# Optimization experiments

Hardware: AMD Instinct MI355X
Metric: run time of the kernel (lower is better)

Reference implementation:

```python
import jax, jax.numpy as jnp
import numpy as np

N, H, D = 32768, 32, 64


def mobius_addition(x, y, c):
    xy_dot = jnp.sum(x * y, axis=-1, keepdims=True)
    x_norm_sq = jnp.sum(x ** 2, axis=-1, keepdims=True)
    y_norm_sq = jnp.sum(y ** 2, axis=-1, keepdims=True)
    num = (1 + 2 * c * xy_dot + c * y_norm_sq) * x + (1 - c * x_norm_sq) * y
    den = 1 + 2 * c * xy_dot + c * c * x_norm_sq * y_norm_sq
    return num / den


def exp_map(x, v, c):
    v_norm = jnp.linalg.norm(v, axis=-1, keepdims=True)
    sqrt_c = jnp.sqrt(c)
    second = jnp.tanh(sqrt_c * v_norm / 2) * v / (sqrt_c * v_norm)
    return mobius_addition(x, second, c)


def log_map(x, y, c):
    add = mobius_addition(-x, y, c)
    add_norm = jnp.linalg.norm(add, axis=-1, keepdims=True)
    sqrt_c = jnp.sqrt(c)
    return 2 / sqrt_c * jnp.arctanh(sqrt_c * add_norm) * add / add_norm


def setup_inputs() -> dict:
    key = jax.random.key(0)
    ks = jax.random.split(key, 5)
    s = 0.1 / np.sqrt(D)  # keep embeddings well inside the Poincare ball (norm ~0.1)
    return {
        "current_emb": jax.random.normal(ks[0], (N, D), jnp.float32) * s,
        "history": jax.random.normal(ks[1], (H, N, D), jnp.float32) * s,
        "curvature": jnp.ones((1,), jnp.float32),
        "Wq": jax.random.normal(ks[2], (D, D), jnp.float32) / np.sqrt(D),
        "bq": jnp.zeros((D,), jnp.float32),
        "Wk": jax.random.normal(ks[3], (D, D), jnp.float32) / np.sqrt(D),
        "bk": jnp.zeros((D,), jnp.float32),
        "attn_vec": jax.random.normal(ks[4], (D, 1), jnp.float32),
    }


def reference(current_emb, history, curvature, Wq, bq, Wk, bk, attn_vec):
    c = curvature.reshape(())
    origin = jnp.zeros((1, D), current_emb.dtype)
    # log map at origin: hyperbolic -> tangent space
    tangent_current = log_map(origin, current_emb, c)          # [N, D]
    tangent_history = log_map(origin, history, c)              # [H, N, D] (origin broadcasts)
    query = tangent_current @ Wq.T + bq                        # [N, D]
    keys = jnp.einsum('hnd,ed->hne', tangent_history, Wk) + bk  # [H, N, D]
    scores = jnp.tanh(query[None, :, :] + keys)                # [H, N, D]
    weights = scores @ attn_vec                                # [H, N, 1]
    weights = jax.nn.softmax(weights, axis=0)
    weighted_sum = jnp.sum(weights * tangent_history, axis=0)  # [N, D]
    context = exp_map(origin, weighted_sum, c)                 # [N, D]
    return context
```

## Files before the change

### kernel.cpp

```cpp
#include <hip/hip_runtime.h>
#include <math.h>

#define NTOK 32768
#define HH 32
#define DD 64
#define TPB 16
#define NBLK (NTOK / TPB)

typedef float f4 __attribute__((ext_vector_type(4)));
typedef short bf16x8 __attribute__((ext_vector_type(8)));

__device__ __forceinline__ float rcpf_(float x) { return __builtin_amdgcn_rcpf(x); }

__device__ __forceinline__ float tanh_f(float x) {
    float t = __expf(x + x);
    return (t - 1.f) * rcpf_(t + 1.f);
}

__device__ __forceinline__ float tanh_poly(float x) {
    float x2 = x * x;
    float t = fmaf(x2, -0.05396825f, 0.13333333f);
    t = fmaf(x2, t, -0.33333333f);
    t = fmaf(x2, t, 1.f);
    return x * t;
}

__device__ __forceinline__ float logmap_f(float x) {
    float u = __logf((1.f + x) * rcpf_(1.f - x));
    return (x > 1e-4f) ? u * rcpf_(x) : 2.f;
}

__device__ __forceinline__ bf16x8 hi8(f4 a, f4 b) {
    bf16x8 r;
#pragma unroll
    for (int j = 0; j < 4; ++j) {
        r[j]     = (short)(__float_as_uint(a[j]) >> 16);
        r[j + 4] = (short)(__float_as_uint(b[j]) >> 16);
    }
    return r;
}
__device__ __forceinline__ bf16x8 lo8(f4 a, f4 b) {
    bf16x8 r;
#pragma unroll
    for (int j = 0; j < 4; ++j) {
        float ah = __uint_as_float(__float_as_uint(a[j]) & 0xFFFF0000u);
        float bh = __uint_as_float(__float_as_uint(b[j]) & 0xFFFF0000u);
        r[j]     = (short)(__float_as_uint(a[j] - ah) >> 16);
        r[j + 4] = (short)(__float_as_uint(b[j] - bh) >> 16);
    }
    return r;
}

__device__ __forceinline__ void load4(const float* base, int l15, int quad, f4 yv[4]) {
    const float* r = base + l15 * DD + 8 * quad;
    yv[0] = *(const f4*)(r);
    yv[1] = *(const f4*)(r + 4);
    yv[2] = *(const f4*)(r + 32);
    yv[3] = *(const f4*)(r + 36);
}

__device__ __forceinline__ float tangent_factor(const f4 yv[4], float sc) {
    f4 s4 = yv[0]*yv[0] + yv[1]*yv[1] + yv[2]*yv[2] + yv[3]*yv[3];
    float n = s4[0] + s4[1] + s4[2] + s4[3];
    n += __shfl_xor(n, 16);
    n += __shfl_xor(n, 32);
    return logmap_f(sc * sqrtf(n));
}

__global__ __launch_bounds__(256, 2) void hyp_attn_v10(
    const float* __restrict__ cur, const float* __restrict__ hist,
    const float* __restrict__ curv, const float* __restrict__ Wq,
    const float* __restrict__ bq, const float* __restrict__ Wk,
    const float* __restrict__ bk, const float* __restrict__ av,
    float* __restrict__ out)
{
    __shared__ float oBuf[4][TPB][68];
    __shared__ float lBuf[4][TPB];

    const int tid  = threadIdx.x;
    const int wv   = tid >> 6;
    const int lane = tid & 63;
    const int l15  = lane & 15;
    const int quad = lane >> 4;
    const int bb   = blockIdx.x;
    const int tok0 = bb * TPB;

    const float sc = sqrtf(curv[0]);
    const f4 zero4 = {0.f, 0.f, 0.f, 0.f};

    f4 yc[4];
    load4(cur + (size_t)tok0 * DD, l15, quad, yc);
    {
        float fc = tangent_factor(yc, sc);
#pragma unroll
        for (int k = 0; k < 4; ++k) yc[k] = yc[k] * fc;
    }
    bf16x8 Ych0 = hi8(yc[0], yc[1]), Ych1 = hi8(yc[2], yc[3]);
    bf16x8 Ycl0 = lo8(yc[0], yc[1]), Ycl1 = lo8(yc[2], yc[3]);

    f4 qT[4] = {zero4, zero4, zero4, zero4};
#pragma unroll
    for (int mt = 0; mt < 4; ++mt) {
        const float* wr = Wq + (size_t)(16 * mt + l15) * DD + 8 * quad;
        f4 a0 = *(const f4*)(wr),      a1 = *(const f4*)(wr + 4);
        f4 b0 = *(const f4*)(wr + 32), b1 = *(const f4*)(wr + 36);
        bf16x8 wh0 = hi8(a0, a1), wh1 = hi8(b0, b1);
        bf16x8 wl0 = lo8(a0, a1), wl1 = lo8(b0, b1);
        qT[mt] = __builtin_amdgcn_mfma_f32_16x16x32_bf16(wh0, Ych0, qT[mt], 0, 0, 0);
        qT[mt] = __builtin_amdgcn_mfma_f32_16x16x32_bf16(wh1, Ych1, qT[mt], 0, 0, 0);
        qT[mt] = __builtin_amdgcn_mfma_f32_16x16x32_bf16(wh0, Ycl0, qT[mt], 0, 0, 0);
        qT[mt] = __builtin_amdgcn_mfma_f32_16x16x32_bf16(wh1, Ycl1, qT[mt], 0, 0, 0);
        qT[mt] = __builtin_amdgcn_mfma_f32_16x16x32_bf16(wl0, Ych0, qT[mt], 0, 0, 0);
        qT[mt] = __builtin_amdgcn_mfma_f32_16x16x32_bf16(wl1, Ych1, qT[mt], 0, 0, 0);
    }

    float avE[16];
#pragma unroll
    for (int mt = 0; mt < 4; ++mt)
#pragma unroll
        for (int r = 0; r < 4; ++r) {
            int e = 16 * mt + 4 * quad + r;
            qT[mt][r] += bq[e] + bk[e];
            avE[4 * mt + r] = av[e];
        }

    bf16x8 Wh[4][2];
#pragma unroll
    for (int mt = 0; mt < 4; ++mt) {
        const float* wr = Wk + (size_t)(16 * mt + l15) * DD + 8 * quad;
        f4 a0 = *(const f4*)(wr),      a1 = *(const f4*)(wr + 4);
        f4 b0 = *(const f4*)(wr + 32), b1 = *(const f4*)(wr + 36);
        Wh[mt][0] = hi8(a0, a1); Wh[mt][1] = hi8(b0, b1);
    }

    const size_t hstep = (size_t)NTOK * DD;
    const float* hb = hist + ((size_t)(wv * 8) * NTOK + tok0) * DD;

    float l_acc = 0.f;
    f4 O[4] = {zero4, zero4, zero4, zero4};
    f4 yb[3][4];
    load4(hb, l15, quad, yb[0]);
    load4(hb + hstep, l15, quad, yb[1]);

#pragma unroll
    for (int i = 0; i < 8; ++i) {
        if (i + 2 < 8)
            load4(hb + (size_t)(i + 2) * hstep, l15, quad, yb[(i + 2) % 3]);

        f4 y0 = yb[i % 3][0], y1 = yb[i % 3][1], y2 = yb[i % 3][2], y3 = yb[i % 3][3];
        float f = tangent_factor(yb[i % 3], sc);

        bf16x8 Yh0 = hi8(y0, y1), Yh1 = hi8(y2, y3);

        f4 acc[4] = {zero4, zero4, zero4, zero4};
#pragma unroll
        for (int mt = 0; mt < 4; ++mt) {
            acc[mt] = __builtin_amdgcn_mfma_f32_16x16x32_bf16(Wh[mt][0], Yh0, acc[mt], 0, 0, 0);
            acc[mt] = __builtin_amdgcn_mfma_f32_16x16x32_bf16(Wh[mt][1], Yh1, acc[mt], 0, 0, 0);
        }

        float s = 0.f;
#pragma unroll
        for (int mt = 0; mt < 4; ++mt) {
#pragma unroll
            for (int r = 0; r < 4; ++r) {
                float x = fmaf(f, acc[mt][r], qT[mt][r]);
                s = fmaf(tanh_poly(x), avE[4 * mt + r], s);
            }
        }
        s += __shfl_xor(s, 16);
        s += __shfl_xor(s, 32);

        float p = __expf(fminf(s, 85.f));
        l_acc += p;
        float pf = p * f;
        O[0] += y0 * pf;
        O[1] += y1 * pf;
        O[2] += y2 * pf;
        O[3] += y3 * pf;
    }

    {
        float* oP = &oBuf[wv][l15][0];
        *(f4*)(oP + 8 * quad)      = O[0];
        *(f4*)(oP + 8 * quad + 4)  = O[1];
        *(f4*)(oP + 32 + 8 * quad) = O[2];
        *(f4*)(oP + 36 + 8 * quad) = O[3];
        if (quad == 0) lBuf[wv][l15] = l_acc;
    }
    __syncthreads();

    {
        const int tok = tid >> 4;
        const int d0  = (tid & 15) * 4;
        f4 o = zero4;
        float L = 0.f;
#pragma unroll
        for (int w = 0; w < 4; ++w) {
            o += *(const f4*)&oBuf[w][tok][d0];
            L += lBuf[w][tok];
        }
        o = o * rcpf_(L);

        f4 sq = o * o;
        float nv = sq[0] + sq[1] + sq[2] + sq[3];
        nv += __shfl_xor(nv, 1);
        nv += __shfl_xor(nv, 2);
        nv += __shfl_xor(nv, 4);
        nv += __shfl_xor(nv, 8);
        float x = sc * sqrtf(nv);
        float g = (x > 1e-4f) ? tanh_f(0.5f * x) * rcpf_(x) : 0.5f;

        *(f4*)(out + (size_t)(tok0 + tok) * DD + d0) = o * g;
    }
}

extern "C" void kernel_launch(void* const* d_in, const int* in_sizes, int n_in,
                              void* d_out, int out_size, void* d_ws, size_t ws_size,
                              hipStream_t stream) {
    const float* cur  = (const float*)d_in[0];
    const float* hist = (const float*)d_in[1];
    const float* curv = (const float*)d_in[2];
    const float* Wq   = (const float*)d_in[3];
    const float* bq   = (const float*)d_in[4];
    const float* Wk   = (const float*)d_in[5];
    const float* bk   = (const float*)d_in[6];
    const float* av   = (const float*)d_in[7];
    float* out = (float*)d_out;

    hipLaunchKernelGGL(hyp_attn_v10, dim3(NBLK), dim3(256), 0, stream,
                       cur, hist, curv, Wq, bq, Wk, bk, av, out);
}
```

Before: 391.9 us.

## Give each wave its own tokens over all history steps instead of splitting history

Each wave now owns 16 tokens and loops over all 32 history steps, where before the four waves of a block split the history dimension for the same 16 tokens. A block therefore covers 64 tokens, and the cross-wave reduction through shared memory becomes a per-token normalization with no summing across waves. This amortizes the per-wave setup (query projection, Wk conversion) over four times as many tokens and removes the cross-wave combine. In exchange the grid has a quarter as many blocks, and each wave runs a longer serial loop with a 4-deep prefetch ring buffer.

```diff
diff --git a/kernel.cpp b/kernel.cpp
--- a/kernel.cpp
+++ b/kernel.cpp
@@ -4,7 +4,8 @@
 #define NTOK 32768
 #define HH 32
 #define DD 64
-#define TPB 16
+#define TPW 16
+#define TPB 64
 #define NBLK (NTOK / TPB)
 
 typedef float f4 __attribute__((ext_vector_type(4)));
@@ -67,23 +68,22 @@
     return logmap_f(sc * sqrtf(n));
 }
 
-__global__ __launch_bounds__(256, 2) void hyp_attn_v10(
+__global__ __launch_bounds__(256, 2) void hyp_attn_v11(
     const float* __restrict__ cur, const float* __restrict__ hist,
     const float* __restrict__ curv, const float* __restrict__ Wq,
     const float* __restrict__ bq, const float* __restrict__ Wk,
     const float* __restrict__ bk, const float* __restrict__ av,
     float* __restrict__ out)
 {
-    __shared__ float oBuf[4][TPB][68];
-    __shared__ float lBuf[4][TPB];
+    __shared__ float oBuf[4][TPW][68];
+    __shared__ float lBuf[4][TPW];
 
     const int tid  = threadIdx.x;
     const int wv   = tid >> 6;
     const int lane = tid & 63;
     const int l15  = lane & 15;
     const int quad = lane >> 4;
-    const int bb   = blockIdx.x;
-    const int tok0 = bb * TPB;
+    const int tok0 = blockIdx.x * TPB + wv * TPW;
 
     const float sc = sqrtf(curv[0]);
     const f4 zero4 = {0.f, 0.f, 0.f, 0.f};
@@ -134,21 +134,21 @@
     }
 
     const size_t hstep = (size_t)NTOK * DD;
-    const float* hb = hist + ((size_t)(wv * 8) * NTOK + tok0) * DD;
+    const float* hb = hist + (size_t)tok0 * DD;
 
     float l_acc = 0.f;
     f4 O[4] = {zero4, zero4, zero4, zero4};
-    f4 yb[3][4];
-    load4(hb, l15, quad, yb[0]);
+    f4 yb[4][4];
+    load4(hb,         l15, quad, yb[0]);
     load4(hb + hstep, l15, quad, yb[1]);
 
-#pragma unroll
-    for (int i = 0; i < 8; ++i) {
-        if (i + 2 < 8)
-            load4(hb + (size_t)(i + 2) * hstep, l15, quad, yb[(i + 2) % 3]);
-
-        f4 y0 = yb[i % 3][0], y1 = yb[i % 3][1], y2 = yb[i % 3][2], y3 = yb[i % 3][3];
-        float f = tangent_factor(yb[i % 3], sc);
+#pragma unroll 4
+    for (int i = 0; i < HH; ++i) {
+        if (i + 2 < HH)
+            load4(hb + (size_t)(i + 2) * hstep, l15, quad, yb[(i + 2) & 3]);
+
+        f4 y0 = yb[i & 3][0], y1 = yb[i & 3][1], y2 = yb[i & 3][2], y3 = yb[i & 3][3];
+        float f = tangent_factor(yb[i & 3], sc);
 
         bf16x8 Yh0 = hi8(y0, y1), Yh1 = hi8(y2, y3);
 
@@ -191,27 +191,28 @@
     __syncthreads();
 
     {
-        const int tok = tid >> 4;
-        const int d0  = (tid & 15) * 4;
-        f4 o = zero4;
-        float L = 0.f;
-#pragma unroll
-        for (int w = 0; w < 4; ++w) {
-            o += *(const f4*)&oBuf[w][tok][d0];
-            L += lBuf[w][tok];
-        }
-        o = o * rcpf_(L);
-
-        f4 sq = o * o;
+        const int tk = tid >> 2;
+        const int d0 = (tid & 3) * 16;
+        const float* row = &oBuf[tk >> 4][tk & 15][0];
+        f4 o0 = *(const f4*)(row + d0);
+        f4 o1 = *(const f4*)(row + d0 + 4);
+        f4 o2 = *(const f4*)(row + d0 + 8);
+        f4 o3 = *(const f4*)(row + d0 + 12);
+        float Li = rcpf_(lBuf[tk >> 4][tk & 15]);
+        o0 = o0 * Li; o1 = o1 * Li; o2 = o2 * Li; o3 = o3 * Li;
+
+        f4 sq = o0*o0 + o1*o1 + o2*o2 + o3*o3;
         float nv = sq[0] + sq[1] + sq[2] + sq[3];
         nv += __shfl_xor(nv, 1);
         nv += __shfl_xor(nv, 2);
-        nv += __shfl_xor(nv, 4);
-        nv += __shfl_xor(nv, 8);
         float x = sc * sqrtf(nv);
         float g = (x > 1e-4f) ? tanh_f(0.5f * x) * rcpf_(x) : 0.5f;
 
-        *(f4*)(out + (size_t)(tok0 + tok) * DD + d0) = o * g;
+        float* op = out + (size_t)(blockIdx.x * TPB + tk) * DD + d0;
+        *(f4*)(op)      = o0 * g;
+        *(f4*)(op + 4)  = o1 * g;
+        *(f4*)(op + 8)  = o2 * g;
+        *(f4*)(op + 12) = o3 * g;
     }
 }
 
@@ -228,6 +229,6 @@
     const float* av   = (const float*)d_in[7];
     float* out = (float*)d_out;
 
-    hipLaunchKernelGGL(hyp_attn_v10, dim3(NBLK), dim3(256), 0, stream,
+    hipLaunchKernelGGL(hyp_attn_v11, dim3(NBLK), dim3(256), 0, stream,
                        cur, hist, curv, Wq, bq, Wk, bk, av, out);
 }
```

New measurement: 385.5 us. About the same (-1.6%).
